# Kernel tuning notes

Measured on AMD Instinct MI355X. Metric: run time of the kernel, lower is better.

The kernel has to match this reference:

```python
import jax, jax.numpy as jnp
import numpy as np

SCALE = 0.08838834764831845  # 1/sqrt(head_dim=128)


def setup_inputs() -> dict:
    key = jax.random.key(0)
    ks = jax.random.split(key, 6)
    B, H, KH, D, S = 16, 32, 8, 128, 8192
    q = jax.random.normal(ks[0], (B, H, D), dtype=jnp.float32)
    k = jax.random.normal(ks[1], (B, KH, D), dtype=jnp.float32)
    v = jax.random.normal(ks[2], (B, KH, D), dtype=jnp.float32)
    k_cache = jax.random.normal(ks[3], (B, S, KH, D), dtype=jnp.float32)
    v_cache = jax.random.normal(ks[4], (B, S, KH, D), dtype=jnp.float32)
    slot_mapping = jax.random.randint(ks[5], (B,), 0, S, dtype=jnp.int64)
    return {"q": q, "k": k, "v": v, "k_cache": k_cache,
            "v_cache": v_cache, "slot_mapping": slot_mapping}


def reference(q, k, v, k_cache, v_cache, slot_mapping):
    # Decode-stage paged attention with GQA.
    # q: [B, H, D]; k,v: [B, KH, D]; caches: [B, S, KH, D]; slot_mapping: [B]
    B, H, D = q.shape
    KH = k.shape[1]
    G = H // KH  # num_queries_per_kv
    b_idx = jnp.arange(B)
    # store_kvcache: scatter new k/v into cache at per-sequence slots
    kc = k_cache.at[b_idx, slot_mapping].set(k)
    vc = v_cache.at[b_idx, slot_mapping].set(v)
    # GQA attention without repeat_interleave: group query heads per kv head
    qg = q.reshape(B, KH, G, D)
    scores = jnp.einsum('bkgd,bskd->bkgs', qg, kc) * SCALE  # [B,KH,G,S]
    w = jax.nn.softmax(scores, axis=-1)
    out = jnp.einsum('bkgs,bskd->bkgd', w, vc)              # [B,KH,G,D]
    return out.reshape(B, H * D)
```

## Files before the change

kernel.cpp:

```cpp
#include <hip/hip_runtime.h>

#define NB 16
#define NH 32
#define NKH 8
#define NG 4
#define ND 128
#define NS 8192
#define ROWF 1024
#define ATT_SCALE 0.08838834764831845f
#define SC2 (0.08838834764831845f * 1.44269504088896340736f)

__device__ __forceinline__ int load_slot(const int* __restrict__ sm, int b) {
    bool is64 = true;
#pragma unroll
    for (int i = 0; i < 8; ++i) is64 = is64 && (sm[2 * i + 1] == 0);
    return is64 ? sm[2 * b] : sm[b];
}

__global__ __launch_bounds__(1024, 4) void attn_fused(
    const float* __restrict__ qin, const float* __restrict__ knew,
    const float* __restrict__ vnew, const float* __restrict__ kc,
    const float* __restrict__ vc, const int* __restrict__ slot_map,
    float* __restrict__ out)
{
    const int bid   = blockIdx.x;
    const int pair  = bid & 127;
    const int dhalf = bid >> 7;
    const int kh = pair & 7;
    const int b  = pair >> 3;
    const int tid  = threadIdx.x;
    const int wave = tid >> 6;
    const int lane = tid & 63;
    const int quarter = lane >> 4;
    const int il   = lane & 15;
    const int dk0  = il * 8;
    const int dv0  = dhalf * 64 + il * 4;

    const int slot = load_slot(slot_map, b);

    float4 qa[NG], qb[NG];
#pragma unroll
    for (int g = 0; g < NG; ++g) {
        const float* qrow = qin + ((size_t)(b * NH + kh * NG + g)) * ND + dk0;
        qa[g] = *(const float4*)(qrow);
        qb[g] = *(const float4*)(qrow + 4);
    }

    const size_t ck0 = (size_t)b * NS * ROWF + (size_t)kh * ND + dk0;
    const size_t cv0 = (size_t)b * NS * ROWF + (size_t)kh * ND + dv0;
    const float* krow_new = knew + ((size_t)(b * NKH + kh)) * ND + dk0;
    const float* vrow_new = vnew + ((size_t)(b * NKH + kh)) * ND + dv0;

    float l[NG];
    float4 acc[NG];
#pragma unroll
    for (int g = 0; g < NG; ++g) {
        l[g] = 0.f;
        acc[g] = make_float4(0.f, 0.f, 0.f, 0.f);
    }

    const int s0 = wave * 4 + quarter;

    int s_cur = s0;
    const float* kp = (s_cur == slot) ? krow_new : (kc + ck0 + (size_t)s_cur * ROWF);
    const float* vp = (s_cur == slot) ? vrow_new : (vc + cv0 + (size_t)s_cur * ROWF);
    float4 ka = ((const float4*)kp)[0];
    float4 kb = ((const float4*)kp)[1];
    float4 vv = *(const float4*)vp;

#pragma unroll 2
    for (int i = 1; i <= NS / 64; ++i) {
        float4 nka, nkb, nvv;
        if (i < NS / 64) {
            const int sn = s0 + i * 64;
            const float* nkp = (sn == slot) ? krow_new : (kc + ck0 + (size_t)sn * ROWF);
            const float* nvp = (sn == slot) ? vrow_new : (vc + cv0 + (size_t)sn * ROWF);
            nka = ((const float4*)nkp)[0];
            nkb = ((const float4*)nkp)[1];
            nvv = *(const float4*)nvp;
        }

        float t[NG];
#pragma unroll
        for (int g = 0; g < NG; ++g) {
            t[g] = ka.x * qa[g].x + ka.y * qa[g].y + ka.z * qa[g].z + ka.w * qa[g].w
                 + kb.x * qb[g].x + kb.y * qb[g].y + kb.z * qb[g].z + kb.w * qb[g].w;
        }
#pragma unroll
        for (int g = 0; g < NG; ++g) t[g] += __shfl_xor(t[g], 8);
#pragma unroll
        for (int g = 0; g < NG; ++g) t[g] += __shfl_xor(t[g], 4);
#pragma unroll
        for (int g = 0; g < NG; ++g) t[g] += __shfl_xor(t[g], 2);
#pragma unroll
        for (int g = 0; g < NG; ++g) t[g] += __shfl_xor(t[g], 1);

#pragma unroll
        for (int g = 0; g < NG; ++g) {
            const float p = exp2f(t[g] * SC2);
            l[g] += p;
            acc[g].x += p * vv.x;
            acc[g].y += p * vv.y;
            acc[g].z += p * vv.z;
            acc[g].w += p * vv.w;
        }

        ka = nka; kb = nkb; vv = nvv;
    }

#pragma unroll
    for (int g = 0; g < NG; ++g) {
        l[g] += __shfl_xor(l[g], 16);
        l[g] += __shfl_xor(l[g], 32);
        acc[g].x += __shfl_xor(acc[g].x, 16); acc[g].x += __shfl_xor(acc[g].x, 32);
        acc[g].y += __shfl_xor(acc[g].y, 16); acc[g].y += __shfl_xor(acc[g].y, 32);
        acc[g].z += __shfl_xor(acc[g].z, 16); acc[g].z += __shfl_xor(acc[g].z, 32);
        acc[g].w += __shfl_xor(acc[g].w, 16); acc[g].w += __shfl_xor(acc[g].w, 32);
    }

    __shared__ float s_acc[16][NG][64];
    __shared__ float s_l[16][NG];
    if (quarter == 0) {
#pragma unroll
        for (int g = 0; g < NG; ++g)
            *(float4*)&s_acc[wave][g][il * 4] = acc[g];
        if (il == 0) {
#pragma unroll
            for (int g = 0; g < NG; ++g) s_l[wave][g] = l[g];
        }
    }
    __syncthreads();

    if (tid < NG * 64) {
        const int g  = tid >> 6;
        const int dd = tid & 63;
        float L = 0.f, o = 0.f;
#pragma unroll
        for (int w = 0; w < 16; ++w) {
            L += s_l[w][g];
            o += s_acc[w][g][dd];
        }
        out[((size_t)(b * NH + kh * NG + g)) * ND + dhalf * 64 + dd] = o / L;
    }
}

extern "C" void kernel_launch(void* const* d_in, const int* in_sizes, int n_in,
                              void* d_out, int out_size, void* d_ws, size_t ws_size,
                              hipStream_t stream) {
    const float* q  = (const float*)d_in[0];
    const float* k  = (const float*)d_in[1];
    const float* v  = (const float*)d_in[2];
    const float* kc = (const float*)d_in[3];
    const float* vc = (const float*)d_in[4];
    const int* slot = (const int*)d_in[5];
    float* out = (float*)d_out;
    (void)d_ws; (void)ws_size; (void)in_sizes; (void)n_in; (void)out_size;

    attn_fused<<<dim3(256), dim3(1024), 0, stream>>>(q, k, v, kc, vc, slot, out);
}
```

Baseline: 190.8 us.

## Split sequence across blocks and merge partial softmax sums in second kernel

Instead of splitting the V head dimension across two blocks, which made both blocks read the full K rows, each block now handles half of the sequence over the full head dimension, so K is read once per pair. Partial unnormalized sums and denominators go to workspace and a small merge kernel combines them. This cuts redundant K traffic at the cost of an extra launch, workspace writes, and more accumulator registers. The original fused kernel remains as a fallback when the workspace is too small.

Result: slower. 211.3 us (+10.7%).

```diff
diff --git a/kernel.cpp b/kernel.cpp
--- a/kernel.cpp
+++ b/kernel.cpp
@@ -15,6 +15,159 @@
 #pragma unroll
     for (int i = 0; i < 8; ++i) is64 = is64 && (sm[2 * i + 1] == 0);
     return is64 ? sm[2 * b] : sm[b];
+}
+
+__global__ __launch_bounds__(1024, 4) void attn_partial(
+    const float* __restrict__ qin, const float* __restrict__ knew,
+    const float* __restrict__ vnew, const float* __restrict__ kc,
+    const float* __restrict__ vc, const int* __restrict__ slot_map,
+    float* __restrict__ wsacc,
+    float* __restrict__ wsl)
+{
+    const int bid   = blockIdx.x;
+    const int shalf = bid & 1;
+    const int pair  = bid >> 1;
+    const int kh = pair & 7;
+    const int b  = pair >> 3;
+    const int tid  = threadIdx.x;
+    const int wave = tid >> 6;
+    const int lane = tid & 63;
+    const int quarter = lane >> 4;
+    const int il   = lane & 15;
+    const int d0   = il * 8;
+
+    const int slot = load_slot(slot_map, b);
+
+    float4 qa[NG], qb[NG];
+#pragma unroll
+    for (int g = 0; g < NG; ++g) {
+        const float* qrow = qin + ((size_t)(b * NH + kh * NG + g)) * ND + d0;
+        qa[g] = *(const float4*)(qrow);
+        qb[g] = *(const float4*)(qrow + 4);
+    }
+
+    const size_t cb = (size_t)b * NS * ROWF + (size_t)kh * ND + d0;
+    const float* krow_new = knew + ((size_t)(b * NKH + kh)) * ND + d0;
+    const float* vrow_new = vnew + ((size_t)(b * NKH + kh)) * ND + d0;
+
+    float l[NG];
+    float4 aca[NG], acb[NG];
+#pragma unroll
+    for (int g = 0; g < NG; ++g) {
+        l[g] = 0.f;
+        aca[g] = make_float4(0.f, 0.f, 0.f, 0.f);
+        acb[g] = make_float4(0.f, 0.f, 0.f, 0.f);
+    }
+
+    const int s0 = shalf * (NS / 2) + wave * 4 + quarter;
+
+    {
+        const float* kp = (s0 == slot) ? krow_new : (kc + cb + (size_t)s0 * ROWF);
+        const float* vp = (s0 == slot) ? vrow_new : (vc + cb + (size_t)s0 * ROWF);
+        float4 ka = ((const float4*)kp)[0];
+        float4 kb = ((const float4*)kp)[1];
+        float4 va = ((const float4*)vp)[0];
+        float4 vb = ((const float4*)vp)[1];
+
+#pragma unroll 2
+        for (int i = 1; i <= NS / 2 / 64; ++i) {
+            float4 nka, nkb, nva, nvb;
+            if (i < NS / 2 / 64) {
+                const int sn = s0 + i * 64;
+                const float* nkp = (sn == slot) ? krow_new : (kc + cb + (size_t)sn * ROWF);
+                const float* nvp = (sn == slot) ? vrow_new : (vc + cb + (size_t)sn * ROWF);
+                nka = ((const float4*)nkp)[0];
+                nkb = ((const float4*)nkp)[1];
+                nva = ((const float4*)nvp)[0];
+                nvb = ((const float4*)nvp)[1];
+            }
+
+            float t[NG];
+#pragma unroll
+            for (int g = 0; g < NG; ++g) {
+                t[g] = ka.x * qa[g].x + ka.y * qa[g].y + ka.z * qa[g].z + ka.w * qa[g].w
+                     + kb.x * qb[g].x + kb.y * qb[g].y + kb.z * qb[g].z + kb.w * qb[g].w;
+            }
+#pragma unroll
+            for (int g = 0; g < NG; ++g) t[g] += __shfl_xor(t[g], 8);
+#pragma unroll
+            for (int g = 0; g < NG; ++g) t[g] += __shfl_xor(t[g], 4);
+#pragma unroll
+            for (int g = 0; g < NG; ++g) t[g] += __shfl_xor(t[g], 2);
+#pragma unroll
+            for (int g = 0; g < NG; ++g) t[g] += __shfl_xor(t[g], 1);
+
+#pragma unroll
+            for (int g = 0; g < NG; ++g) {
+                const float p = exp2f(t[g] * SC2);
+                l[g] += p;
+                aca[g].x += p * va.x; aca[g].y += p * va.y;
+                aca[g].z += p * va.z; aca[g].w += p * va.w;
+                acb[g].x += p * vb.x; acb[g].y += p * vb.y;
+                acb[g].z += p * vb.z; acb[g].w += p * vb.w;
+            }
+
+            ka = nka; kb = nkb; va = nva; vb = nvb;
+        }
+    }
+
+#pragma unroll
+    for (int g = 0; g < NG; ++g) {
+        l[g] += __shfl_xor(l[g], 16);
+        l[g] += __shfl_xor(l[g], 32);
+        aca[g].x += __shfl_xor(aca[g].x, 16); aca[g].x += __shfl_xor(aca[g].x, 32);
+        aca[g].y += __shfl_xor(aca[g].y, 16); aca[g].y += __shfl_xor(aca[g].y, 32);
+        aca[g].z += __shfl_xor(aca[g].z, 16); aca[g].z += __shfl_xor(aca[g].z, 32);
+        aca[g].w += __shfl_xor(aca[g].w, 16); aca[g].w += __shfl_xor(aca[g].w, 32);
+        acb[g].x += __shfl_xor(acb[g].x, 16); acb[g].x += __shfl_xor(acb[g].x, 32);
+        acb[g].y += __shfl_xor(acb[g].y, 16); acb[g].y += __shfl_xor(acb[g].y, 32);
+        acb[g].z += __shfl_xor(acb[g].z, 16); acb[g].z += __shfl_xor(acb[g].z, 32);
+        acb[g].w += __shfl_xor(acb[g].w, 16); acb[g].w += __shfl_xor(acb[g].w, 32);
+    }
+
+    __shared__ float s_acc[16][NG][ND];
+    __shared__ float s_l[16][NG];
+    if (quarter == 0) {
+#pragma unroll
+        for (int g = 0; g < NG; ++g) {
+            *(float4*)&s_acc[wave][g][d0]     = aca[g];
+            *(float4*)&s_acc[wave][g][d0 + 4] = acb[g];
+        }
+        if (il == 0) {
+#pragma unroll
+            for (int g = 0; g < NG; ++g) s_l[wave][g] = l[g];
+        }
+    }
+    __syncthreads();
+
+    if (tid < NG * ND) {
+        const int g  = tid >> 7;
+        const int dd = tid & 127;
+        float L = 0.f, o = 0.f;
+#pragma unroll
+        for (int w = 0; w < 16; ++w) {
+            L += s_l[w][g];
+            o += s_acc[w][g][dd];
+        }
+        wsacc[((size_t)bid * NG + g) * ND + dd] = o;
+        if (dd == 0) wsl[bid * NG + g] = L;
+    }
+}
+
+__global__ __launch_bounds__(512) void attn_merge(
+    const float* __restrict__ wsacc, const float* __restrict__ wsl,
+    float* __restrict__ out)
+{
+    const int pair = blockIdx.x;
+    const int kh = pair & 7;
+    const int b  = pair >> 3;
+    const int tid = threadIdx.x;
+    const int g  = tid >> 7;
+    const int dd = tid & 127;
+    const float o = wsacc[((size_t)(pair * 2) * NG + g) * ND + dd]
+                  + wsacc[((size_t)(pair * 2 + 1) * NG + g) * ND + dd];
+    const float L = wsl[(pair * 2) * NG + g] + wsl[(pair * 2 + 1) * NG + g];
+    out[((size_t)(b * NH + kh * NG + g)) * ND + dd] = o / L;
 }
 
 __global__ __launch_bounds__(1024, 4) void attn_fused(
@@ -60,10 +213,8 @@
     }
 
     const int s0 = wave * 4 + quarter;
-
-    int s_cur = s0;
-    const float* kp = (s_cur == slot) ? krow_new : (kc + ck0 + (size_t)s_cur * ROWF);
-    const float* vp = (s_cur == slot) ? vrow_new : (vc + cv0 + (size_t)s_cur * ROWF);
+    const float* kp = (s0 == slot) ? krow_new : (kc + ck0 + (size_t)s0 * ROWF);
+    const float* vp = (s0 == slot) ? vrow_new : (vc + cv0 + (size_t)s0 * ROWF);
     float4 ka = ((const float4*)kp)[0];
     float4 kb = ((const float4*)kp)[1];
     float4 vv = *(const float4*)vp;
@@ -79,7 +230,6 @@
             nkb = ((const float4*)nkp)[1];
             nvv = *(const float4*)nvp;
         }
-
         float t[NG];
 #pragma unroll
         for (int g = 0; g < NG; ++g) {
@@ -94,17 +244,13 @@
         for (int g = 0; g < NG; ++g) t[g] += __shfl_xor(t[g], 2);
 #pragma unroll
         for (int g = 0; g < NG; ++g) t[g] += __shfl_xor(t[g], 1);
-
 #pragma unroll
         for (int g = 0; g < NG; ++g) {
             const float p = exp2f(t[g] * SC2);
             l[g] += p;
-            acc[g].x += p * vv.x;
-            acc[g].y += p * vv.y;
-            acc[g].z += p * vv.z;
-            acc[g].w += p * vv.w;
-        }
-
+            acc[g].x += p * vv.x; acc[g].y += p * vv.y;
+            acc[g].z += p * vv.z; acc[g].w += p * vv.w;
+        }
         ka = nka; kb = nkb; vv = nvv;
     }
 
@@ -154,7 +300,16 @@
     const float* vc = (const float*)d_in[4];
     const int* slot = (const int*)d_in[5];
     float* out = (float*)d_out;
-    (void)d_ws; (void)ws_size; (void)in_sizes; (void)n_in; (void)out_size;
-
-    attn_fused<<<dim3(256), dim3(1024), 0, stream>>>(q, k, v, kc, vc, slot, out);
-}
+    (void)in_sizes; (void)n_in; (void)out_size;
+
+    const size_t need = ((size_t)256 * NG * ND + 256 * NG) * sizeof(float);
+    if (ws_size >= need) {
+        float* wsacc = (float*)d_ws;
+        float* wsl   = wsacc + (size_t)256 * NG * ND;
+        attn_partial<<<dim3(256), dim3(1024), 0, stream>>>(
+            q, k, v, kc, vc, slot, wsacc, wsl);
+        attn_merge<<<dim3(128), dim3(512), 0, stream>>>(wsacc, wsl, out);
+    } else {
+        attn_fused<<<dim3(256), dim3(1024), 0, stream>>>(q, k, v, kc, vc, slot, out);
+    }
+}
```
